# Optimization experiments

Hardware: AMD Instinct MI355X
Metric: run time of the kernel (lower is better)

Reference implementation:

```python
import jax, jax.numpy as jnp
import numpy as np

S = 2048      # max_seq_len
D_IN = 2048   # input dim
H = 16        # num query heads
KVH = 4       # kv heads (GQA branch)
HD = 128      # per-head embedding dim
D_OUT = 2048
THETA = 10000.0


def rope(x):
    # x: [S, h, d]. Matches eqx.nn.RotaryPositionalEmbedding (GPT-NeoX style):
    # cos/sin of outer(t, inv_freq) tiled over the two halves, rotate_half = (-x2, x1).
    s, h, d = x.shape
    inv_freq = 1.0 / (THETA ** (jnp.arange(0, d, 2, dtype=jnp.float32) / d))  # [d/2]
    t = jnp.arange(s, dtype=jnp.float32)
    freqs = jnp.outer(t, inv_freq)                         # [S, d/2]
    cos = jnp.tile(jnp.cos(freqs), (1, 2))[:, None, :]     # [S, 1, d]
    sin = jnp.tile(jnp.sin(freqs), (1, 2))[:, None, :]
    x1, x2 = jnp.split(x, 2, axis=-1)
    rot = jnp.concatenate((-x2, x1), axis=-1)
    return x * cos + rot * sin


def setup_inputs() -> dict:
    key = jax.random.key(0)
    k0, k1, k2, k3, k4 = jax.random.split(key, 5)
    lim_in = 1.0 / np.sqrt(D_IN).astype(np.float32)
    lim_o = 1.0 / np.sqrt(H * HD).astype(np.float32)
    x = jax.random.normal(k0, (S, D_IN), jnp.float32)
    Wq = jax.random.uniform(k1, (H * HD, D_IN), jnp.float32, -lim_in, lim_in)
    Wk = jax.random.uniform(k2, (KVH * HD, D_IN), jnp.float32, -lim_in, lim_in)
    Wv = jax.random.uniform(k3, (KVH * HD, D_IN), jnp.float32, -lim_in, lim_in)
    Wo = jax.random.uniform(k4, (D_OUT, H * HD), jnp.float32, -lim_o, lim_o)
    return {"x": x, "Wq": Wq, "Wk": Wk, "Wv": Wv, "Wo": Wo}


def reference(x, Wq, Wk, Wv, Wo):
    # Projections (eqx Linear, no bias: y = W @ x)
    q = (x @ Wq.T).reshape(S, H, HD)
    k = (x @ Wk.T).reshape(S, KVH, HD)
    v = (x @ Wv.T).reshape(S, KVH, HD)
    q = rope(q)
    k = rope(k)
    mask = jnp.tril(jnp.ones((S, S), dtype=bool))           # causal
    scale = 1.0 / jnp.sqrt(jnp.asarray(HD, q.dtype))
    # GQA branch: every query head attends against every kv head separately
    logits = jnp.einsum('shd,SHd->hHsS', q * scale, k)      # [H=16, KVH=4, S, S]
    logits = jnp.where(mask, logits, jnp.finfo(logits.dtype).min)
    w = jax.nn.softmax(logits, axis=-1)
    attn = jnp.einsum('hHsS,SHd->shd', w, v) / KVH          # mean over kv heads
    return attn.reshape(S, H * HD) @ Wo.T
```

## Files before the change

kernel.cpp:

```cpp
#include <hip/hip_runtime.h>

#define SEQ 2048
#define DIN 2048
#define NH 16
#define NKVH 4
#define DH 128
#define NQ 2048
#define QSCALE2 0.1275174684f

typedef unsigned short ushort_t;
typedef unsigned int uint_t;
typedef __attribute__((ext_vector_type(8))) __bf16 bf16x8;
typedef __attribute__((ext_vector_type(8))) unsigned short ushort8;
typedef __attribute__((ext_vector_type(4))) float f32x4;
typedef __attribute__((ext_vector_type(16))) float f32x16;

#if __has_builtin(__builtin_amdgcn_exp2f)
#define EXP2(x) __builtin_amdgcn_exp2f(x)
#else
#define EXP2(x) exp2f(x)
#endif

__device__ __forceinline__ float b2f(ushort_t u){ return __uint_as_float(((unsigned int)u)<<16); }
__device__ __forceinline__ ushort_t f2b(float f){
  unsigned int u = __float_as_uint(f);
  u += 0x7fff + ((u>>16)&1);
  return (ushort_t)(u>>16);
}
__device__ __forceinline__ f32x4 mfma16(bf16x8 a, bf16x8 b, f32x4 c){
  return __builtin_amdgcn_mfma_f32_16x16x32_bf16(a, b, c, 0, 0, 0);
}
__device__ __forceinline__ f32x16 mfma32(bf16x8 a, bf16x8 b, f32x16 c){
  return __builtin_amdgcn_mfma_f32_32x32x16_bf16(a, b, c, 0, 0, 0);
}
__device__ __forceinline__ void gload16(const void* g, void* l){
  __builtin_amdgcn_global_load_lds((__attribute__((address_space(1))) void*)(void*)g,
                                   (__attribute__((address_space(3))) void*)l, 16, 0, 0);
}
__device__ __forceinline__ f32x16 zero16(){
  f32x16 z = {0.f,0.f,0.f,0.f,0.f,0.f,0.f,0.f,0.f,0.f,0.f,0.f,0.f,0.f,0.f,0.f};
  return z;
}

__global__ void detect_bf16(const ushort_t* __restrict__ wq, int* __restrict__ flag){
  __shared__ int any_big;
  if (threadIdx.x==0) any_big = 0;
  __syncthreads();
  int big = 0;
  for (int i=threadIdx.x; i<4096; i+=256){
    float v = b2f(wq[i]);
    if (!(fabsf(v) < 1.0f)) big = 1;
  }
  if (big) atomicOr(&any_big, 1);
  __syncthreads();
  if (threadIdx.x==0) flag[0] = any_big ? 0 : 1;
}

__global__ __launch_bounds__(256)
void cvt_all(const void* __restrict__ x, const void* __restrict__ wq,
             const void* __restrict__ wk, const void* __restrict__ wv,
             const void* __restrict__ wo,
             ushort_t* __restrict__ xb, ushort_t* __restrict__ wqb,
             ushort_t* __restrict__ wkb, ushort_t* __restrict__ wvb,
             ushort_t* __restrict__ wob, const int* __restrict__ flag){
  int b = blockIdx.x;
  const void* src; ushort_t* dst; int off;
  if      (b < 2048){ src=x;  dst=xb;  off=b; }
  else if (b < 4096){ src=wq; dst=wqb; off=b-2048; }
  else if (b < 4608){ src=wk; dst=wkb; off=b-4096; }
  else if (b < 5120){ src=wv; dst=wvb; off=b-4608; }
  else              { src=wo; dst=wob; off=b-5120; }
  const int i = (off*256 + threadIdx.x)*8;
  if (flag[0]){
    *(ushort8*)&dst[i] = *(const ushort8*)((const ushort_t*)src + i);
  } else {
    f32x4 a = *(const f32x4*)((const float*)src + i);
    f32x4 c = *(const f32x4*)((const float*)src + i + 4);
    ushort8 w;
    #pragma unroll
    for (int e=0;e<4;e++){ w[e]=f2b(a[e]); w[4+e]=f2b(c[e]); }
    *(ushort8*)&dst[i] = w;
  }
}

__global__ __launch_bounds__(256)
void sum4(const ushort_t* __restrict__ pb, ushort_t* __restrict__ ab){
  const size_t PS = (size_t)SEQ*NQ;
  const int i = (blockIdx.x*256 + threadIdx.x)*8;
  ushort8 a = *(const ushort8*)&pb[i];
  ushort8 b = *(const ushort8*)&pb[PS + i];
  ushort8 c = *(const ushort8*)&pb[2*PS + i];
  ushort8 d = *(const ushort8*)&pb[3*PS + i];
  ushort8 w;
  #pragma unroll
  for (int e=0;e<8;e++)
    w[e] = f2b((b2f(a[e]) + b2f(b[e])) + (b2f(c[e]) + b2f(d[e])));
  *(ushort8*)&ab[i] = w;
}

__device__ __forceinline__ void stage128x32(const ushort_t* src, int ld, char* ldsbase, int tid){
  #pragma unroll
  for (int p=0;p<2;p++){
    int lin = p*4096 + tid*16;
    int r = lin>>6, cb = lin&63;
    gload16(src + (size_t)r*ld + (cb>>1), ldsbase + p*4096 + ((tid>>6)<<10));
  }
}
__device__ __forceinline__ void stage64x32(const ushort_t* src, int ld, char* ldsbase, int tid){
  int lin = tid*16;
  int r = lin>>6, cb = lin&63;
  gload16(src + (size_t)r*ld + (cb>>1), ldsbase + ((tid>>6)<<10));
}

__global__ __launch_bounds__(256, 3)
void gemm_qkv(const ushort_t* __restrict__ X, const ushort_t* __restrict__ Wq,
              const ushort_t* __restrict__ Wk, const ushort_t* __restrict__ Wv,
              ushort_t* __restrict__ qb, ushort_t* __restrict__ kb,
              ushort_t* __restrict__ vb){
  __shared__ __attribute__((aligned(16))) ushort_t lds_a[2][64*32];
  __shared__ __attribute__((aligned(16))) ushort_t lds_b[2][128*32];
  const int tid = threadIdx.x;
  const int wid = tid>>6, lane = tid&63;
  const int lhi = lane>>4, llo = lane&15;
  const int flat = blockIdx.x;
  const int wf = (flat & 7)*96 + (flat >> 3);
  const int mb = (wf & 31)*64;
  const int ny = wf >> 5;
  const ushort_t* W = (ny < 16) ? (Wq + (size_t)ny*128*DIN)
                    : (ny < 20) ? (Wk + (size_t)(ny-16)*128*DIN)
                    : (Wv + (size_t)(ny-20)*128*DIN);
  const int wr = (wid>>1)*32, wc = (wid&1)*64;

  f32x4 acc[2][4];
  #pragma unroll
  for (int i=0;i<2;i++)
    #pragma unroll
    for (int j=0;j<4;j++) acc[i][j] = (f32x4){0.f,0.f,0.f,0.f};

  auto stage = [&](int b, int t){
    stage64x32 (X + (size_t)mb*DIN + t*32, DIN, (char*)lds_a[b], tid);
    stage128x32(W + t*32, DIN, (char*)lds_b[b], tid);
  };

  stage(0, 0);
  __syncthreads();
  int cur = 0;
  for (int t=0; t<64; ++t){
    if (t < 63) stage(cur^1, t+1);
    bf16x8 af[2], bfr[4];
    #pragma unroll
    for (int i=0;i<2;i++) af[i]  = *(const bf16x8*)&lds_a[cur][(wr+i*16+llo)*32 + lhi*8];
    #pragma unroll
    for (int j=0;j<4;j++) bfr[j] = *(const bf16x8*)&lds_b[cur][(wc+j*16+llo)*32 + lhi*8];
    __builtin_amdgcn_s_setprio(1);
    #pragma unroll
    for (int i=0;i<2;i++)
      #pragma unroll
      for (int j=0;j<4;j++)
        acc[i][j] = mfma16(af[i], bfr[j], acc[i][j]);
    __builtin_amdgcn_s_setprio(0);
    __syncthreads();
    cur ^= 1;
  }
  #pragma unroll
  for (int i=0;i<2;i++)
    #pragma unroll
    for (int j=0;j<4;j++)
      #pragma unroll
      for (int rr=0;rr<4;rr++){
        int s  = mb + wr + i*16 + lhi*4 + rr;
        int nl = wc + j*16 + llo;
        ushort_t val = f2b(acc[i][j][rr]);
        if (ny < 16)      qb[(size_t)s*NQ + ny*128 + nl] = val;
        else if (ny < 20) kb[(size_t)(ny-16)*SEQ*DH + (size_t)s*DH + nl] = val;
        else              vb[(size_t)(ny-20)*SEQ*DH + (size_t)s*DH + nl] = val;
      }
}

__global__ __launch_bounds__(256, 2)
void gemm_plain_b16(const ushort_t* __restrict__ A, const ushort_t* __restrict__ Wo,
                    void* __restrict__ out, const int* __restrict__ flag){
  __shared__ __attribute__((aligned(16))) ushort_t lds_a[2][128*32];
  __shared__ __attribute__((aligned(16))) ushort_t lds_b[2][64*32];
  const int isb = flag[0];
  const int tid = threadIdx.x;
  const int wid = tid>>6, lane = tid&63;
  const int lhi = lane>>4, llo = lane&15;
  const int flat = blockIdx.x;
  const int wf = (flat & 7)*64 + (flat >> 3);
  const int mb = (wf & 15)*128;
  const int nb = (wf >> 4)*64;
  const int wr = (wid>>1)*64, wc = (wid&1)*32;

  f32x4 acc[4][2];
  #pragma unroll
  for (int i=0;i<4;i++)
    #pragma unroll
    for (int j=0;j<2;j++) acc[i][j] = (f32x4){0.f,0.f,0.f,0.f};

  auto stage = [&](int b, int t){
    stage128x32(A  + (size_t)mb*NQ + t*32, NQ, (char*)lds_a[b], tid);
    stage64x32 (Wo + (size_t)nb*NQ + t*32, NQ, (char*)lds_b[b], tid);
  };

  stage(0, 0);
  __syncthreads();
  int cur = 0;
  for (int t=0; t<64; ++t){
    if (t < 63) stage(cur^1, t+1);
    bf16x8 af[4], bfr[2];
    #pragma unroll
    for (int i=0;i<4;i++) af[i]  = *(const bf16x8*)&lds_a[cur][(wr+i*16+llo)*32 + lhi*8];
    #pragma unroll
    for (int j=0;j<2;j++) bfr[j] = *(const bf16x8*)&lds_b[cur][(wc+j*16+llo)*32 + lhi*8];
    __builtin_amdgcn_s_setprio(1);
    #pragma unroll
    for (int i=0;i<4;i++)
      #pragma unroll
      for (int j=0;j<2;j++)
        acc[i][j] = mfma16(af[i], bfr[j], acc[i][j]);
    __builtin_amdgcn_s_setprio(0);
    __syncthreads();
    cur ^= 1;
  }
  #pragma unroll
  for (int i=0;i<4;i++)
    #pragma unroll
    for (int j=0;j<2;j++)
      #pragma unroll
      for (int rr=0;rr<4;rr++){
        int s  = mb + wr + i*16 + lhi*4 + rr;
        int nl = nb + wc + j*16 + llo;
        float v = acc[i][j][rr];
        if (isb) ((ushort_t*)out)[(size_t)s*NQ + nl] = f2b(v);
        else     ((float*)out)[(size_t)s*NQ + nl] = v;
      }
}

__global__ __launch_bounds__(256, 2)
void gemm_plain_f32(const float* __restrict__ A, const ushort_t* __restrict__ Wo,
                    void* __restrict__ out, const int* __restrict__ flag){
  __shared__ __attribute__((aligned(16))) ushort_t lds_a[2][128*32];
  __shared__ __attribute__((aligned(16))) ushort_t lds_b[2][128*32];
  const int isb = flag[0];
  const int tid = threadIdx.x;
  const int wid = tid>>6, lane = tid&63;
  const int lhi = lane>>4, llo = lane&15;
  const int mb = blockIdx.x*128;
  const int nb = blockIdx.y*128;
  const int wr = (wid>>1)*64, wc = (wid&1)*64;
  const int r = tid>>1, c0 = (tid&1)*16;
  const float* Ab = A + (size_t)(mb+r)*NQ + c0;

  f32x4 acc[4][4];
  #pragma unroll
  for (int i=0;i<4;i++)
    #pragma unroll
    for (int j=0;j<4;j++) acc[i][j] = (f32x4){0.f,0.f,0.f,0.f};

  f32x4 raf[4];
  auto ldA = [&](int t){
    raf[0] = *(const f32x4*)(Ab + t*32);
    raf[1] = *(const f32x4*)(Ab + t*32 + 4);
    raf[2] = *(const f32x4*)(Ab + t*32 + 8);
    raf[3] = *(const f32x4*)(Ab + t*32 + 12);
  };
  auto stA = [&](ushort_t* lds){
    ushort8 w0, w1;
    #pragma unroll
    for (int e=0;e<4;e++){ w0[e]=f2b(raf[0][e]); w0[4+e]=f2b(raf[1][e]);
                           w1[e]=f2b(raf[2][e]); w1[4+e]=f2b(raf[3][e]); }
    *(ushort8*)&lds[r*32+c0]   = w0;
    *(ushort8*)&lds[r*32+c0+8] = w1;
  };

  ldA(0);
  stage128x32(Wo + (size_t)nb*NQ, NQ, (char*)lds_b[0], tid);
  stA(lds_a[0]);
  __syncthreads();
  int cur = 0;
  for (int t=0; t<64; ++t){
    const bool more = (t < 63);
    if (more){
      ldA(t+1);
      stage128x32(Wo + (size_t)nb*NQ + (t+1)*32, NQ, (char*)lds_b[cur^1], tid);
    }
    bf16x8 af[4], bfr[4];
    #pragma unroll
    for (int i=0;i<4;i++) af[i]  = *(const bf16x8*)&lds_a[cur][(wr+i*16+llo)*32 + lhi*8];
    #pragma unroll
    for (int j=0;j<4;j++) bfr[j] = *(const bf16x8*)&lds_b[cur][(wc+j*16+llo)*32 + lhi*8];
    __builtin_amdgcn_s_setprio(1);
    #pragma unroll
    for (int i=0;i<4;i++)
      #pragma unroll
      for (int j=0;j<4;j++)
        acc[i][j] = mfma16(af[i], bfr[j], acc[i][j]);
    __builtin_amdgcn_s_setprio(0);
    if (more) stA(lds_a[cur^1]);
    __syncthreads();
    cur ^= 1;
  }
  #pragma unroll
  for (int i=0;i<4;i++)
    #pragma unroll
    for (int j=0;j<4;j++)
      #pragma unroll
      for (int rr=0;rr<4;rr++){
        int s  = mb + wr + i*16 + lhi*4 + rr;
        int nl = nb + wc + j*16 + llo;
        float v = acc[i][j][rr];
        if (isb) ((ushort_t*)out)[(size_t)s*NQ + nl] = f2b(v);
        else     ((float*)out)[(size_t)s*NQ + nl] = v;
      }
}

__global__ __launch_bounds__(256)
void rope_all(ushort_t* __restrict__ qbuf, ushort_t* __restrict__ kbuf){
  int idx = blockIdx.x*256 + threadIdx.x;
  ushort_t* buf; int head_stride, row_stride; float scale;
  if (idx < 16*SEQ*64){ buf=qbuf; head_stride=DH; row_stride=NQ; scale=QSCALE2; }
  else { idx -= 16*SEQ*64; buf=kbuf; head_stride=SEQ*DH; row_stride=DH; scale=1.0f; }
  const int j = idx & 63;
  const int s = (idx>>6) & (SEQ-1);
  const int h = idx>>17;
  const size_t a1 = (size_t)h*head_stride + (size_t)s*row_stride + j;
  const size_t a2 = a1 + 64;
  const float inv = __expf((float)j * -0.1439115683f);
  const float ang = (float)s * inv;
  const float c = cosf(ang), sn = sinf(ang);
  const float x1 = b2f(buf[a1]), x2 = b2f(buf[a2]);
  buf[a1] = f2b((x1*c - x2*sn)*scale);
  buf[a2] = f2b((x2*c + x1*sn)*scale);
}

__global__ __launch_bounds__(256)
void vtrans(const ushort_t* __restrict__ vb, ushort_t* __restrict__ vt){
  __shared__ __attribute__((aligned(16))) ushort_t tile[64*72];
  const int tid = threadIdx.x;
  const int kv = blockIdx.z, s0 = blockIdx.x*64, d0 = blockIdx.y*64;
  #pragma unroll
  for (int p=0;p<2;p++){
    int lin = p*4096 + tid*16;
    int rr = lin>>7, cb = lin&127;
    ushort8 val = *(const ushort8*)&vb[(size_t)kv*SEQ*DH + (size_t)(s0+rr)*DH + d0 + (cb>>1)];
    *(ushort8*)&tile[rr*72 + (cb>>1)] = val;
  }
  __syncthreads();
  #pragma unroll
  for (int p=0;p<2;p++){
    int lin = p*4096 + tid*16;
    int rr = lin>>7, cb = lin&127;
    int cc = cb>>1;
    ushort8 val;
    #pragma unroll
    for (int e=0;e<8;e++) val[e] = tile[(cc+e)*72 + rr];
    *(ushort8*)&vt[(size_t)kv*DH*SEQ + (size_t)(d0+rr)*SEQ + s0 + cc] = val;
  }
}

__global__ __launch_bounds__(256, 2)
void attn_kernel(const ushort_t* __restrict__ qb, const ushort_t* __restrict__ kb,
                 const ushort_t* __restrict__ vt, float* __restrict__ abf,
                 ushort_t* __restrict__ pb, int use_pb){
  __shared__ __attribute__((aligned(16))) ushort_t lds_k[64*128];
  __shared__ __attribute__((aligned(16))) ushort_t lds_v[128*64];
  __shared__ float lsum[4][32];
  const int tid = threadIdx.x;
  const int wid = tid>>6, lane = tid&63;
  const int l31 = lane&31, hi = lane>>5;
  const int flat = (int)(blockIdx.x + 16*blockIdx.y + 256*blockIdx.z);
  const int xcd = flat & 7, slot = flat >> 3;
  const int kv = xcd >> 1;
  const int idx = slot*2 + (xcd & 1);
  const int g = idx >> 4, h = idx & 15;
  const int t = (g<4) ? 15-g : (g<8) ? 4+g : (g<12) ? g-4 : 15-g;
  const ushort_t* kbase = kb + (size_t)kv*SEQ*DH;
  const ushort_t* vbase = vt + (size_t)kv*DH*SEQ;
  const int NKT = 2*t + 2;
  const int qrow0 = t*128 + wid*32;
  const int qg = qrow0 + l31;

  bf16x8 qf[8];
  {
    const ushort_t* qp = qb + (size_t)qg*NQ + h*DH + hi*8;
    #pragma unroll
    for (int ks=0;ks<8;ks++) qf[ks] = *(const bf16x8*)(qp + ks*16);
  }
  f32x16 oacc[4];
  #pragma unroll
  for (int d=0;d<4;d++) oacc[d] = zero16();
  float psum = 0.f;

  for (int kt=0; kt<NKT; ++kt){
    __syncthreads();
    #pragma unroll
    for (int pp=0;pp<4;pp++){
      int lin = pp*4096 + tid*16;
      int rk = lin>>8, cbk = lin&255;
      int sck = cbk ^ ((rk&15)<<4);
      gload16(kbase + (size_t)(kt*64 + rk)*DH + (sck>>1), (char*)lds_k + pp*4096 + (wid<<10));
      int rv = lin>>7, cbv = lin&127;
      int scv = cbv ^ ((rv&7)<<4);
      gload16(vbase + (size_t)rv*SEQ + kt*64 + (scv>>1), (char*)lds_v + pp*4096 + (wid<<10));
    }
    __syncthreads();

    #pragma unroll
    for (int ss=0;ss<2;ss++){
      const int kvb = kt*64 + ss*32;
      if (kvb > qrow0 + 31) continue;
      f32x16 sacc = zero16();
      #pragma unroll
      for (int ks=0;ks<8;ks++){
        int row = ss*32 + l31;
        int boff = row*256 + ((ks*32 + hi*16) ^ ((row&15)<<4));
        bf16x8 kf = *(const bf16x8*)((const char*)lds_k + boff);
        sacc = mfma32(kf, qf[ks], sacc);
      }
      const bool edge = (kvb + 31 > qrow0);
      #pragma unroll
      for (int rr=0; rr<16; rr++){
        float e = EXP2(sacc[rr]);
        if (edge){
          int kvg = kvb + (rr&3) + 8*(rr>>2) + 4*hi;
          if (kvg > qg) e = 0.f;
        }
        sacc[rr] = e;
        psum += e;
      }
      #pragma unroll
      for (int pk=0; pk<2; pk++){
        uint_t P0, P1, P2, P3;
        asm("v_cvt_pk_bf16_f32 %0, %1, %2" : "=v"(P0) : "v"(sacc[8*pk+0]), "v"(sacc[8*pk+1]));
        asm("v_cvt_pk_bf16_f32 %0, %1, %2" : "=v"(P1) : "v"(sacc[8*pk+2]), "v"(sacc[8*pk+3]));
        asm("v_cvt_pk_bf16_f32 %0, %1, %2" : "=v"(P2) : "v"(sacc[8*pk+4]), "v"(sacc[8*pk+5]));
        asm("v_cvt_pk_bf16_f32 %0, %1, %2" : "=v"(P3) : "v"(sacc[8*pk+6]), "v"(sacc[8*pk+7]));
        asm("v_permlane32_swap_b32 %0, %1" : "+v"(P0), "+v"(P2));
        asm("v_permlane32_swap_b32 %0, %1" : "+v"(P1), "+v"(P3));
        uint4 fu; fu.x = P0; fu.y = P1; fu.z = P2; fu.w = P3;
        bf16x8 pf = *(bf16x8*)&fu;
        #pragma unroll
        for (int d=0; d<4; d++){
          int rowv = d*32 + l31;
          int bv = rowv*128 + ((ss*64 + pk*32 + hi*16) ^ ((rowv&7)<<4));
          bf16x8 vf = *(const bf16x8*)((const char*)lds_v + bv);
          oacc[d] = mfma32(pf, vf, oacc[d]);
        }
      }
    }
  }

  {
    float tot = psum + __shfl_xor(psum, 32);
    lsum[wid][l31] = tot;
    if (use_pb){
      ushort_t* pbk = pb + (size_t)kv*SEQ*NQ + (size_t)h*DH;
      #pragma unroll
      for (int rr=0; rr<16; rr++){
        int qr = (rr&3) + 8*(rr>>2) + 4*hi;
        float sc = 0.25f / lsum[wid][qr];
        #pragma unroll
        for (int d=0; d<4; d++)
          pbk[(size_t)(qrow0 + qr)*NQ + d*32 + l31] = f2b(oacc[d][rr]*sc);
      }
    } else {
      #pragma unroll
      for (int rr=0; rr<16; rr++){
        int qr = (rr&3) + 8*(rr>>2) + 4*hi;
        float sc = 0.25f / lsum[wid][qr];
        #pragma unroll
        for (int d=0; d<4; d++)
          atomicAdd(&abf[(size_t)(qrow0 + qr)*NQ + h*DH + d*32 + l31], oacc[d][rr]*sc);
      }
    }
  }
}

extern "C" void kernel_launch(void* const* d_in, const int* in_sizes, int n_in,
                              void* d_out, int out_size, void* d_ws, size_t ws_size,
                              hipStream_t stream) {
  const void* x  = d_in[0];
  const void* wq = d_in[1];
  const void* wk = d_in[2];
  const void* wv = d_in[3];
  const void* wo = d_in[4];
  char* ws = (char*)d_ws;
  const bool big_ws = (ws_size >= ((size_t)55<<20));

  if (big_ws){
    ushort_t* qbuf = (ushort_t*)(ws);
    ushort_t* kbuf = (ushort_t*)(ws + ((size_t)8<<20));
    ushort_t* vbuf = (ushort_t*)(ws + ((size_t)10<<20));
    ushort_t* vtb  = (ushort_t*)(ws + ((size_t)12<<20));
    ushort_t* pbuf = (ushort_t*)(ws + ((size_t)14<<20));
    ushort_t* xb   = (ushort_t*)(ws + ((size_t)14<<20));
    ushort_t* wqb  = (ushort_t*)(ws + ((size_t)22<<20));
    ushort_t* wkb  = (ushort_t*)(ws + ((size_t)30<<20));
    ushort_t* wvb  = (ushort_t*)(ws + ((size_t)32<<20));
    ushort_t* wob  = (ushort_t*)(ws + ((size_t)46<<20));
    ushort_t* ab   = qbuf;
    int* flag      = (int*)(ws + ((size_t)54<<20));

    hipLaunchKernelGGL(detect_bf16, dim3(1), dim3(256), 0, stream, (const ushort_t*)wq, flag);
    hipLaunchKernelGGL(cvt_all, dim3(7168), dim3(256), 0, stream, x, wq, wk, wv, wo,
                       xb, wqb, wkb, wvb, wob, flag);
    hipLaunchKernelGGL(gemm_qkv, dim3(768), dim3(256), 0, stream, xb, wqb, wkb, wvb, qbuf, kbuf, vbuf);
    hipLaunchKernelGGL(rope_all, dim3(10240), dim3(256), 0, stream, qbuf, kbuf);
    hipLaunchKernelGGL(vtrans, dim3(32,2,4), dim3(256), 0, stream, vbuf, vtb);
    hipLaunchKernelGGL(attn_kernel, dim3(16,16,4), dim3(256), 0, stream, qbuf, kbuf, vtb,
                       (float*)nullptr, pbuf, 1);
    hipLaunchKernelGGL(sum4, dim3(2048), dim3(256), 0, stream, pbuf, ab);
    hipLaunchKernelGGL(gemm_plain_b16, dim3(512), dim3(256), 0, stream, ab, wob, d_out, flag);
  } else {
    ushort_t* qbuf = (ushort_t*)(ws);
    ushort_t* kbuf = (ushort_t*)(ws + ((size_t)8<<20));
    ushort_t* vbuf = (ushort_t*)(ws + ((size_t)10<<20));
    ushort_t* vtb  = (ushort_t*)(ws + ((size_t)12<<20));
    float*    abf  = (float*)(ws + ((size_t)14<<20));
    ushort_t* xb   = (ushort_t*)(ws + ((size_t)14<<20));
    ushort_t* wqb  = (ushort_t*)(ws + ((size_t)22<<20));
    ushort_t* wkb  = (ushort_t*)(ws + ((size_t)30<<20));
    ushort_t* wvb  = (ushort_t*)(ws + ((size_t)32<<20));
    ushort_t* wob  = (ushort_t*)(ws + ((size_t)34<<20));
    int* flag      = (int*)(ws + ((size_t)42<<20));

    hipLaunchKernelGGL(detect_bf16, dim3(1), dim3(256), 0, stream, (const ushort_t*)wq, flag);
    hipLaunchKernelGGL(cvt_all, dim3(7168), dim3(256), 0, stream, x, wq, wk, wv, wo,
                       xb, wqb, wkb, wvb, wob, flag);
    hipLaunchKernelGGL(gemm_qkv, dim3(768), dim3(256), 0, stream, xb, wqb, wkb, wvb, qbuf, kbuf, vbuf);
    hipMemsetAsync(abf, 0, (size_t)SEQ*NQ*sizeof(float), stream);
    hipLaunchKernelGGL(rope_all, dim3(10240), dim3(256), 0, stream, qbuf, kbuf);
    hipLaunchKernelGGL(vtrans, dim3(32,2,4), dim3(256), 0, stream, vbuf, vtb);
    hipLaunchKernelGGL(attn_kernel, dim3(16,16,4), dim3(256), 0, stream, qbuf, kbuf, vtb,
                       abf, (ushort_t*)nullptr, 0);
    hipLaunchKernelGGL(gemm_plain_f32, dim3(16,16), dim3(256), 0, stream, abf, wob, d_out, flag);
  }
}
```

Measured before the change: 204.1 us.

## Fuse RoPE and V transpose into QKV GEMM epilogue, tweak attention and tile order

The QKV GEMM epilogue now stages its tile in LDS to apply RoPE (with the query scale) directly before writing Q and K, and writes V already transposed. This removes the separate rope_all and vtrans kernels along with their global memory round trips. The attention QK loop is split into two independent accumulators to increase MFMA ILP, and the mask check is hoisted out of the exp loop. The output GEMM block-to-tile mapping is also changed for different XCD locality. The costs are extra LDS in gemm_qkv, which may reduce occupancy, and uncoalesced 8-byte stores for the transposed V.

```diff
diff --git a/kernel.cpp b/kernel.cpp
--- a/kernel.cpp
+++ b/kernel.cpp
@@ -12,6 +12,7 @@
 typedef unsigned int uint_t;
 typedef __attribute__((ext_vector_type(8))) __bf16 bf16x8;
 typedef __attribute__((ext_vector_type(8))) unsigned short ushort8;
+typedef __attribute__((ext_vector_type(4))) unsigned short ushort4_t;
 typedef __attribute__((ext_vector_type(4))) float f32x4;
 typedef __attribute__((ext_vector_type(16))) float f32x16;
 
@@ -116,9 +117,10 @@
 void gemm_qkv(const ushort_t* __restrict__ X, const ushort_t* __restrict__ Wq,
               const ushort_t* __restrict__ Wk, const ushort_t* __restrict__ Wv,
               ushort_t* __restrict__ qb, ushort_t* __restrict__ kb,
-              ushort_t* __restrict__ vb){
+              ushort_t* __restrict__ vt){
   __shared__ __attribute__((aligned(16))) ushort_t lds_a[2][64*32];
   __shared__ __attribute__((aligned(16))) ushort_t lds_b[2][128*32];
+  __shared__ __attribute__((aligned(16))) ushort_t lds_e[64*136];
   const int tid = threadIdx.x;
   const int wid = tid>>6, lane = tid&63;
   const int lhi = lane>>4, llo = lane&15;
@@ -162,19 +164,54 @@
     __syncthreads();
     cur ^= 1;
   }
-  #pragma unroll
-  for (int i=0;i<2;i++)
-    #pragma unroll
-    for (int j=0;j<4;j++)
-      #pragma unroll
-      for (int rr=0;rr<4;rr++){
-        int s  = mb + wr + i*16 + lhi*4 + rr;
-        int nl = wc + j*16 + llo;
-        ushort_t val = f2b(acc[i][j][rr]);
-        if (ny < 16)      qb[(size_t)s*NQ + ny*128 + nl] = val;
-        else if (ny < 20) kb[(size_t)(ny-16)*SEQ*DH + (size_t)s*DH + nl] = val;
-        else              vb[(size_t)(ny-20)*SEQ*DH + (size_t)s*DH + nl] = val;
-      }
+
+  if (ny < 20){
+    #pragma unroll
+    for (int i=0;i<2;i++)
+      #pragma unroll
+      for (int j=0;j<4;j++)
+        #pragma unroll
+        for (int rr=0;rr<4;rr++){
+          int sl = wr + i*16 + lhi*4 + rr;
+          int c  = wc + j*16 + llo;
+          lds_e[sl*136 + c] = f2b(acc[i][j][rr]);
+        }
+    __syncthreads();
+    const float scale = (ny < 16) ? QSCALE2 : 1.0f;
+    #pragma unroll
+    for (int i=0;i<2;i++)
+      #pragma unroll
+      for (int j=0;j<4;j++)
+        #pragma unroll
+        for (int rr=0;rr<4;rr++){
+          int sl = wr + i*16 + lhi*4 + rr;
+          int c  = wc + j*16 + llo;
+          int s  = mb + sl;
+          float v1 = acc[i][j][rr];
+          float v2 = b2f(lds_e[sl*136 + (c^64)]);
+          int j6 = c & 63;
+          float inv = __expf((float)j6 * -0.1439115683f);
+          float ang = (float)s * inv;
+          float cth = cosf(ang), sth = sinf(ang);
+          float outv = (c < 64) ? (v1*cth - v2*sth) : (v1*cth + v2*sth);
+          ushort_t val = f2b(outv*scale);
+          if (ny < 16) qb[(size_t)s*NQ + ny*128 + c] = val;
+          else         kb[(size_t)(ny-16)*SEQ*DH + (size_t)s*DH + c] = val;
+        }
+  } else {
+    const size_t vbase = (size_t)(ny-20)*DH*SEQ;
+    #pragma unroll
+    for (int i=0;i<2;i++)
+      #pragma unroll
+      for (int j=0;j<4;j++){
+        int d = wc + j*16 + llo;
+        int s = mb + wr + i*16 + lhi*4;
+        ushort4_t w;
+        #pragma unroll
+        for (int rr=0;rr<4;rr++) w[rr] = f2b(acc[i][j][rr]);
+        *(ushort4_t*)&vt[vbase + (size_t)d*SEQ + s] = w;
+      }
+  }
 }
 
 __global__ __launch_bounds__(256, 2)
@@ -187,9 +224,9 @@
   const int wid = tid>>6, lane = tid&63;
   const int lhi = lane>>4, llo = lane&15;
   const int flat = blockIdx.x;
-  const int wf = (flat & 7)*64 + (flat >> 3);
-  const int mb = (wf & 15)*128;
-  const int nb = (wf >> 4)*64;
+  const int xcd = flat & 7, slot = flat >> 3;
+  const int mb = (xcd*2 + (slot>>5))*128;
+  const int nb = (slot&31)*64;
   const int wr = (wid>>1)*64, wc = (wid&1)*32;
 
   f32x4 acc[4][2];
@@ -313,50 +350,6 @@
         if (isb) ((ushort_t*)out)[(size_t)s*NQ + nl] = f2b(v);
         else     ((float*)out)[(size_t)s*NQ + nl] = v;
       }
-}
-
-__global__ __launch_bounds__(256)
-void rope_all(ushort_t* __restrict__ qbuf, ushort_t* __restrict__ kbuf){
-  int idx = blockIdx.x*256 + threadIdx.x;
-  ushort_t* buf; int head_stride, row_stride; float scale;
-  if (idx < 16*SEQ*64){ buf=qbuf; head_stride=DH; row_stride=NQ; scale=QSCALE2; }
-  else { idx -= 16*SEQ*64; buf=kbuf; head_stride=SEQ*DH; row_stride=DH; scale=1.0f; }
-  const int j = idx & 63;
-  const int s = (idx>>6) & (SEQ-1);
-  const int h = idx>>17;
-  const size_t a1 = (size_t)h*head_stride + (size_t)s*row_stride + j;
-  const size_t a2 = a1 + 64;
-  const float inv = __expf((float)j * -0.1439115683f);
-  const float ang = (float)s * inv;
-  const float c = cosf(ang), sn = sinf(ang);
-  const float x1 = b2f(buf[a1]), x2 = b2f(buf[a2]);
-  buf[a1] = f2b((x1*c - x2*sn)*scale);
-  buf[a2] = f2b((x2*c + x1*sn)*scale);
-}
-
-__global__ __launch_bounds__(256)
-void vtrans(const ushort_t* __restrict__ vb, ushort_t* __restrict__ vt){
-  __shared__ __attribute__((aligned(16))) ushort_t tile[64*72];
-  const int tid = threadIdx.x;
-  const int kv = blockIdx.z, s0 = blockIdx.x*64, d0 = blockIdx.y*64;
-  #pragma unroll
-  for (int p=0;p<2;p++){
-    int lin = p*4096 + tid*16;
-    int rr = lin>>7, cb = lin&127;
-    ushort8 val = *(const ushort8*)&vb[(size_t)kv*SEQ*DH + (size_t)(s0+rr)*DH + d0 + (cb>>1)];
-    *(ushort8*)&tile[rr*72 + (cb>>1)] = val;
-  }
-  __syncthreads();
-  #pragma unroll
-  for (int p=0;p<2;p++){
-    int lin = p*4096 + tid*16;
-    int rr = lin>>7, cb = lin&127;
-    int cc = cb>>1;
-    ushort8 val;
-    #pragma unroll
-    for (int e=0;e<8;e++) val[e] = tile[(cc+e)*72 + rr];
-    *(ushort8*)&vt[(size_t)kv*DH*SEQ + (size_t)(d0+rr)*SEQ + s0 + cc] = val;
-  }
 }
 
 __global__ __launch_bounds__(256, 2)
@@ -410,24 +403,33 @@
     for (int ss=0;ss<2;ss++){
       const int kvb = kt*64 + ss*32;
       if (kvb > qrow0 + 31) continue;
-      f32x16 sacc = zero16();
-      #pragma unroll
-      for (int ks=0;ks<8;ks++){
+      f32x16 sacc = zero16(), sacc1 = zero16();
+      #pragma unroll
+      for (int ks=0;ks<8;ks+=2){
         int row = ss*32 + l31;
-        int boff = row*256 + ((ks*32 + hi*16) ^ ((row&15)<<4));
-        bf16x8 kf = *(const bf16x8*)((const char*)lds_k + boff);
-        sacc = mfma32(kf, qf[ks], sacc);
-      }
+        bf16x8 kf0 = *(const bf16x8*)((const char*)lds_k + row*256 + (((ks  )*32 + hi*16) ^ ((row&15)<<4)));
+        bf16x8 kf1 = *(const bf16x8*)((const char*)lds_k + row*256 + (((ks+1)*32 + hi*16) ^ ((row&15)<<4)));
+        sacc  = mfma32(kf0, qf[ks],   sacc);
+        sacc1 = mfma32(kf1, qf[ks+1], sacc1);
+      }
+      sacc = sacc + sacc1;
       const bool edge = (kvb + 31 > qrow0);
-      #pragma unroll
-      for (int rr=0; rr<16; rr++){
-        float e = EXP2(sacc[rr]);
-        if (edge){
+      if (edge){
+        #pragma unroll
+        for (int rr=0; rr<16; rr++){
+          float e = EXP2(sacc[rr]);
           int kvg = kvb + (rr&3) + 8*(rr>>2) + 4*hi;
           if (kvg > qg) e = 0.f;
+          sacc[rr] = e;
+          psum += e;
         }
-        sacc[rr] = e;
-        psum += e;
+      } else {
+        #pragma unroll
+        for (int rr=0; rr<16; rr++){
+          float e = EXP2(sacc[rr]);
+          sacc[rr] = e;
+          psum += e;
+        }
       }
       #pragma unroll
       for (int pk=0; pk<2; pk++){
@@ -491,7 +493,6 @@
   if (big_ws){
     ushort_t* qbuf = (ushort_t*)(ws);
     ushort_t* kbuf = (ushort_t*)(ws + ((size_t)8<<20));
-    ushort_t* vbuf = (ushort_t*)(ws + ((size_t)10<<20));
     ushort_t* vtb  = (ushort_t*)(ws + ((size_t)12<<20));
     ushort_t* pbuf = (ushort_t*)(ws + ((size_t)14<<20));
     ushort_t* xb   = (ushort_t*)(ws + ((size_t)14<<20));
@@ -505,9 +506,7 @@
     hipLaunchKernelGGL(detect_bf16, dim3(1), dim3(256), 0, stream, (const ushort_t*)wq, flag);
     hipLaunchKernelGGL(cvt_all, dim3(7168), dim3(256), 0, stream, x, wq, wk, wv, wo,
                        xb, wqb, wkb, wvb, wob, flag);
-    hipLaunchKernelGGL(gemm_qkv, dim3(768), dim3(256), 0, stream, xb, wqb, wkb, wvb, qbuf, kbuf, vbuf);
-    hipLaunchKernelGGL(rope_all, dim3(10240), dim3(256), 0, stream, qbuf, kbuf);
-    hipLaunchKernelGGL(vtrans, dim3(32,2,4), dim3(256), 0, stream, vbuf, vtb);
+    hipLaunchKernelGGL(gemm_qkv, dim3(768), dim3(256), 0, stream, xb, wqb, wkb, wvb, qbuf, kbuf, vtb);
     hipLaunchKernelGGL(attn_kernel, dim3(16,16,4), dim3(256), 0, stream, qbuf, kbuf, vtb,
                        (float*)nullptr, pbuf, 1);
     hipLaunchKernelGGL(sum4, dim3(2048), dim3(256), 0, stream, pbuf, ab);
@@ -515,7 +514,6 @@
   } else {
     ushort_t* qbuf = (ushort_t*)(ws);
     ushort_t* kbuf = (ushort_t*)(ws + ((size_t)8<<20));
-    ushort_t* vbuf = (ushort_t*)(ws + ((size_t)10<<20));
     ushort_t* vtb  = (ushort_t*)(ws + ((size_t)12<<20));
     float*    abf  = (float*)(ws + ((size_t)14<<20));
     ushort_t* xb   = (ushort_t*)(ws + ((size_t)14<<20));
@@ -528,10 +526,8 @@
     hipLaunchKernelGGL(detect_bf16, dim3(1), dim3(256), 0, stream, (const ushort_t*)wq, flag);
     hipLaunchKernelGGL(cvt_all, dim3(7168), dim3(256), 0, stream, x, wq, wk, wv, wo,
                        xb, wqb, wkb, wvb, wob, flag);
-    hipLaunchKernelGGL(gemm_qkv, dim3(768), dim3(256), 0, stream, xb, wqb, wkb, wvb, qbuf, kbuf, vbuf);
+    hipLaunchKernelGGL(gemm_qkv, dim3(768), dim3(256), 0, stream, xb, wqb, wkb, wvb, qbuf, kbuf, vtb);
     hipMemsetAsync(abf, 0, (size_t)SEQ*NQ*sizeof(float), stream);
-    hipLaunchKernelGGL(rope_all, dim3(10240), dim3(256), 0, stream, qbuf, kbuf);
-    hipLaunchKernelGGL(vtrans, dim3(32,2,4), dim3(256), 0, stream, vbuf, vtb);
     hipLaunchKernelGGL(attn_kernel, dim3(16,16,4), dim3(256), 0, stream, qbuf, kbuf, vtb,
                        abf, (ushort_t*)nullptr, 0);
     hipLaunchKernelGGL(gemm_plain_f32, dim3(16,16), dim3(256), 0, stream, abf, wob, d_out, flag);
```

Measured after the change: 535.8 us. +162.6%, slower.

## Fuse V transpose into QKV GEMM epilogue and partial-sum into output GEMM

Applied to the files above, without the earlier changes.

The QKV GEMM now writes V directly in transposed [kv][d][s] layout with 4-wide vector stores, removing the separate vtrans kernel. The output projection GEMM loads the four bf16 partial attention buffers through registers, sums them, and stores the bf16 result to LDS, replacing the separate sum4 kernel and its intermediate buffer. The block-to-tile mapping of the output GEMM is also changed to group row tiles per XCD. This removes two launches and their global round trips, at the cost of non-async register staging of A and four times the A-operand global reads inside the GEMM.

```diff
diff --git a/kernel.cpp b/kernel.cpp
--- a/kernel.cpp
+++ b/kernel.cpp
@@ -12,6 +12,7 @@
 typedef unsigned int uint_t;
 typedef __attribute__((ext_vector_type(8))) __bf16 bf16x8;
 typedef __attribute__((ext_vector_type(8))) unsigned short ushort8;
+typedef __attribute__((ext_vector_type(4))) unsigned short ushort4_t;
 typedef __attribute__((ext_vector_type(4))) float f32x4;
 typedef __attribute__((ext_vector_type(16))) float f32x16;
 
@@ -83,21 +84,6 @@
   }
 }
 
-__global__ __launch_bounds__(256)
-void sum4(const ushort_t* __restrict__ pb, ushort_t* __restrict__ ab){
-  const size_t PS = (size_t)SEQ*NQ;
-  const int i = (blockIdx.x*256 + threadIdx.x)*8;
-  ushort8 a = *(const ushort8*)&pb[i];
-  ushort8 b = *(const ushort8*)&pb[PS + i];
-  ushort8 c = *(const ushort8*)&pb[2*PS + i];
-  ushort8 d = *(const ushort8*)&pb[3*PS + i];
-  ushort8 w;
-  #pragma unroll
-  for (int e=0;e<8;e++)
-    w[e] = f2b((b2f(a[e]) + b2f(b[e])) + (b2f(c[e]) + b2f(d[e])));
-  *(ushort8*)&ab[i] = w;
-}
-
 __device__ __forceinline__ void stage128x32(const ushort_t* src, int ld, char* ldsbase, int tid){
   #pragma unroll
   for (int p=0;p<2;p++){
@@ -116,7 +102,7 @@
 void gemm_qkv(const ushort_t* __restrict__ X, const ushort_t* __restrict__ Wq,
               const ushort_t* __restrict__ Wk, const ushort_t* __restrict__ Wv,
               ushort_t* __restrict__ qb, ushort_t* __restrict__ kb,
-              ushort_t* __restrict__ vb){
+              ushort_t* __restrict__ vt){
   __shared__ __attribute__((aligned(16))) ushort_t lds_a[2][64*32];
   __shared__ __attribute__((aligned(16))) ushort_t lds_b[2][128*32];
   const int tid = threadIdx.x;
@@ -162,35 +148,52 @@
     __syncthreads();
     cur ^= 1;
   }
-  #pragma unroll
-  for (int i=0;i<2;i++)
-    #pragma unroll
-    for (int j=0;j<4;j++)
-      #pragma unroll
-      for (int rr=0;rr<4;rr++){
-        int s  = mb + wr + i*16 + lhi*4 + rr;
-        int nl = wc + j*16 + llo;
-        ushort_t val = f2b(acc[i][j][rr]);
-        if (ny < 16)      qb[(size_t)s*NQ + ny*128 + nl] = val;
-        else if (ny < 20) kb[(size_t)(ny-16)*SEQ*DH + (size_t)s*DH + nl] = val;
-        else              vb[(size_t)(ny-20)*SEQ*DH + (size_t)s*DH + nl] = val;
-      }
+  if (ny < 20){
+    #pragma unroll
+    for (int i=0;i<2;i++)
+      #pragma unroll
+      for (int j=0;j<4;j++)
+        #pragma unroll
+        for (int rr=0;rr<4;rr++){
+          int s  = mb + wr + i*16 + lhi*4 + rr;
+          int nl = wc + j*16 + llo;
+          ushort_t val = f2b(acc[i][j][rr]);
+          if (ny < 16) qb[(size_t)s*NQ + ny*128 + nl] = val;
+          else         kb[(size_t)(ny-16)*SEQ*DH + (size_t)s*DH + nl] = val;
+        }
+  } else {
+    const size_t vbase = (size_t)(ny-20)*DH*SEQ;
+    #pragma unroll
+    for (int i=0;i<2;i++)
+      #pragma unroll
+      for (int j=0;j<4;j++){
+        int d = wc + j*16 + llo;
+        int s = mb + wr + i*16 + lhi*4;
+        ushort4_t w;
+        #pragma unroll
+        for (int rr=0;rr<4;rr++) w[rr] = f2b(acc[i][j][rr]);
+        *(ushort4_t*)&vt[vbase + (size_t)d*SEQ + s] = w;
+      }
+  }
 }
 
 __global__ __launch_bounds__(256, 2)
-void gemm_plain_b16(const ushort_t* __restrict__ A, const ushort_t* __restrict__ Wo,
-                    void* __restrict__ out, const int* __restrict__ flag){
+void gemm_plain_pb(const ushort_t* __restrict__ pb, const ushort_t* __restrict__ Wo,
+                   void* __restrict__ out, const int* __restrict__ flag){
   __shared__ __attribute__((aligned(16))) ushort_t lds_a[2][128*32];
   __shared__ __attribute__((aligned(16))) ushort_t lds_b[2][64*32];
+  const size_t PS = (size_t)SEQ*NQ;
   const int isb = flag[0];
   const int tid = threadIdx.x;
   const int wid = tid>>6, lane = tid&63;
   const int lhi = lane>>4, llo = lane&15;
   const int flat = blockIdx.x;
-  const int wf = (flat & 7)*64 + (flat >> 3);
-  const int mb = (wf & 15)*128;
-  const int nb = (wf >> 4)*64;
+  const int xcd = flat & 7, slot = flat >> 3;
+  const int mb = (xcd*2 + (slot>>5))*128;
+  const int nb = (slot&31)*64;
   const int wr = (wid>>1)*64, wc = (wid&1)*32;
+  const int r = tid>>1, c0 = (tid&1)*16;
+  const ushort_t* Ab = pb + (size_t)(mb+r)*NQ + c0;
 
   f32x4 acc[4][2];
   #pragma unroll
@@ -198,16 +201,36 @@
     #pragma unroll
     for (int j=0;j<2;j++) acc[i][j] = (f32x4){0.f,0.f,0.f,0.f};
 
-  auto stage = [&](int b, int t){
-    stage128x32(A  + (size_t)mb*NQ + t*32, NQ, (char*)lds_a[b], tid);
-    stage64x32 (Wo + (size_t)nb*NQ + t*32, NQ, (char*)lds_b[b], tid);
+  ushort8 ra[4][2];
+  auto ldA = [&](int t){
+    #pragma unroll
+    for (int k=0;k<4;k++){
+      ra[k][0] = *(const ushort8*)(Ab + (size_t)k*PS + t*32);
+      ra[k][1] = *(const ushort8*)(Ab + (size_t)k*PS + t*32 + 8);
+    }
   };
-
-  stage(0, 0);
+  auto stA = [&](ushort_t* lds){
+    ushort8 w0, w1;
+    #pragma unroll
+    for (int e=0;e<8;e++){
+      w0[e] = f2b((b2f(ra[0][0][e]) + b2f(ra[1][0][e])) + (b2f(ra[2][0][e]) + b2f(ra[3][0][e])));
+      w1[e] = f2b((b2f(ra[0][1][e]) + b2f(ra[1][1][e])) + (b2f(ra[2][1][e]) + b2f(ra[3][1][e])));
+    }
+    *(ushort8*)&lds[r*32+c0]   = w0;
+    *(ushort8*)&lds[r*32+c0+8] = w1;
+  };
+
+  ldA(0);
+  stage64x32(Wo + (size_t)nb*NQ, NQ, (char*)lds_b[0], tid);
+  stA(lds_a[0]);
   __syncthreads();
   int cur = 0;
   for (int t=0; t<64; ++t){
-    if (t < 63) stage(cur^1, t+1);
+    const bool more = (t < 63);
+    if (more){
+      ldA(t+1);
+      stage64x32(Wo + (size_t)nb*NQ + (t+1)*32, NQ, (char*)lds_b[cur^1], tid);
+    }
     bf16x8 af[4], bfr[2];
     #pragma unroll
     for (int i=0;i<4;i++) af[i]  = *(const bf16x8*)&lds_a[cur][(wr+i*16+llo)*32 + lhi*8];
@@ -220,6 +243,7 @@
       for (int j=0;j<2;j++)
         acc[i][j] = mfma16(af[i], bfr[j], acc[i][j]);
     __builtin_amdgcn_s_setprio(0);
+    if (more) stA(lds_a[cur^1]);
     __syncthreads();
     cur ^= 1;
   }
@@ -332,31 +356,6 @@
   const float x1 = b2f(buf[a1]), x2 = b2f(buf[a2]);
   buf[a1] = f2b((x1*c - x2*sn)*scale);
   buf[a2] = f2b((x2*c + x1*sn)*scale);
-}
-
-__global__ __launch_bounds__(256)
-void vtrans(const ushort_t* __restrict__ vb, ushort_t* __restrict__ vt){
-  __shared__ __attribute__((aligned(16))) ushort_t tile[64*72];
-  const int tid = threadIdx.x;
-  const int kv = blockIdx.z, s0 = blockIdx.x*64, d0 = blockIdx.y*64;
-  #pragma unroll
-  for (int p=0;p<2;p++){
-    int lin = p*4096 + tid*16;
-    int rr = lin>>7, cb = lin&127;
-    ushort8 val = *(const ushort8*)&vb[(size_t)kv*SEQ*DH + (size_t)(s0+rr)*DH + d0 + (cb>>1)];
-    *(ushort8*)&tile[rr*72 + (cb>>1)] = val;
-  }
-  __syncthreads();
-  #pragma unroll
-  for (int p=0;p<2;p++){
-    int lin = p*4096 + tid*16;
-    int rr = lin>>7, cb = lin&127;
-    int cc = cb>>1;
-    ushort8 val;
-    #pragma unroll
-    for (int e=0;e<8;e++) val[e] = tile[(cc+e)*72 + rr];
-    *(ushort8*)&vt[(size_t)kv*DH*SEQ + (size_t)(d0+rr)*SEQ + s0 + cc] = val;
-  }
 }
 
 __global__ __launch_bounds__(256, 2)
@@ -491,7 +490,6 @@
   if (big_ws){
     ushort_t* qbuf = (ushort_t*)(ws);
     ushort_t* kbuf = (ushort_t*)(ws + ((size_t)8<<20));
-    ushort_t* vbuf = (ushort_t*)(ws + ((size_t)10<<20));
     ushort_t* vtb  = (ushort_t*)(ws + ((size_t)12<<20));
     ushort_t* pbuf = (ushort_t*)(ws + ((size_t)14<<20));
     ushort_t* xb   = (ushort_t*)(ws + ((size_t)14<<20));
@@ -499,23 +497,19 @@
     ushort_t* wkb  = (ushort_t*)(ws + ((size_t)30<<20));
     ushort_t* wvb  = (ushort_t*)(ws + ((size_t)32<<20));
     ushort_t* wob  = (ushort_t*)(ws + ((size_t)46<<20));
-    ushort_t* ab   = qbuf;
     int* flag      = (int*)(ws + ((size_t)54<<20));
 
     hipLaunchKernelGGL(detect_bf16, dim3(1), dim3(256), 0, stream, (const ushort_t*)wq, flag);
     hipLaunchKernelGGL(cvt_all, dim3(7168), dim3(256), 0, stream, x, wq, wk, wv, wo,
                        xb, wqb, wkb, wvb, wob, flag);
-    hipLaunchKernelGGL(gemm_qkv, dim3(768), dim3(256), 0, stream, xb, wqb, wkb, wvb, qbuf, kbuf, vbuf);
+    hipLaunchKernelGGL(gemm_qkv, dim3(768), dim3(256), 0, stream, xb, wqb, wkb, wvb, qbuf, kbuf, vtb);
     hipLaunchKernelGGL(rope_all, dim3(10240), dim3(256), 0, stream, qbuf, kbuf);
-    hipLaunchKernelGGL(vtrans, dim3(32,2,4), dim3(256), 0, stream, vbuf, vtb);
     hipLaunchKernelGGL(attn_kernel, dim3(16,16,4), dim3(256), 0, stream, qbuf, kbuf, vtb,
                        (float*)nullptr, pbuf, 1);
-    hipLaunchKernelGGL(sum4, dim3(2048), dim3(256), 0, stream, pbuf, ab);
-    hipLaunchKernelGGL(gemm_plain_b16, dim3(512), dim3(256), 0, stream, ab, wob, d_out, flag);
+    hipLaunchKernelGGL(gemm_plain_pb, dim3(512), dim3(256), 0, stream, pbuf, wob, d_out, flag);
   } else {
     ushort_t* qbuf = (ushort_t*)(ws);
     ushort_t* kbuf = (ushort_t*)(ws + ((size_t)8<<20));
-    ushort_t* vbuf = (ushort_t*)(ws + ((size_t)10<<20));
     ushort_t* vtb  = (ushort_t*)(ws + ((size_t)12<<20));
     float*    abf  = (float*)(ws + ((size_t)14<<20));
     ushort_t* xb   = (ushort_t*)(ws + ((size_t)14<<20));
@@ -528,10 +522,9 @@
     hipLaunchKernelGGL(detect_bf16, dim3(1), dim3(256), 0, stream, (const ushort_t*)wq, flag);
     hipLaunchKernelGGL(cvt_all, dim3(7168), dim3(256), 0, stream, x, wq, wk, wv, wo,
                        xb, wqb, wkb, wvb, wob, flag);
-    hipLaunchKernelGGL(gemm_qkv, dim3(768), dim3(256), 0, stream, xb, wqb, wkb, wvb, qbuf, kbuf, vbuf);
+    hipLaunchKernelGGL(gemm_qkv, dim3(768), dim3(256), 0, stream, xb, wqb, wkb, wvb, qbuf, kbuf, vtb);
     hipMemsetAsync(abf, 0, (size_t)SEQ*NQ*sizeof(float), stream);
     hipLaunchKernelGGL(rope_all, dim3(10240), dim3(256), 0, stream, qbuf, kbuf);
-    hipLaunchKernelGGL(vtrans, dim3(32,2,4), dim3(256), 0, stream, vbuf, vtb);
     hipLaunchKernelGGL(attn_kernel, dim3(16,16,4), dim3(256), 0, stream, qbuf, kbuf, vtb,
                        abf, (ushort_t*)nullptr, 0);
     hipLaunchKernelGGL(gemm_plain_f32, dim3(16,16), dim3(256), 0, stream, abf, wob, d_out, flag);
```

Measured after the change: 245.4 us. 20.3% more time.
